# Kernel optimization log

Hardware: AMD Instinct MI355X
Metric: run time of the kernel (lower is better)

The kernel has to match this reference:

```python
import jax, jax.numpy as jnp
import numpy as np

H, HKV, D, HID, T = 16, 4, 128, 2048, 4096
THETA = 10000.0
EPS = 1e-5
NEG = -1e30


def setup_inputs() -> dict:
    key = jax.random.key(0)
    ks = jax.random.split(key, 4)
    return {
        "positions": jnp.arange(T, dtype=jnp.int32),
        "hidden_states": jax.random.normal(ks[0], (T, HID), jnp.float32),
        "w_qkv": jax.random.normal(ks[1], ((H + 2 * HKV) * D, HID), jnp.float32) * 0.02,
        "w_o": jax.random.normal(ks[2], (HID, H * D), jnp.float32) * 0.02,
        "q_norm_w": jnp.ones((H * D,), jnp.float32),
        "k_norm_w": jnp.ones((HKV * D,), jnp.float32),
    }


def _rope(pos, x):
    # x: [T, nh, D]; neox-style rotary over full head_dim
    half = D // 2
    inv_freq = 1.0 / (THETA ** (jnp.arange(0, D, 2, dtype=jnp.float32) / D))  # [D/2]
    ang = pos.astype(jnp.float32)[:, None] * inv_freq  # [T, D/2]
    cos = jnp.cos(ang)[:, None, :]
    sin = jnp.sin(ang)[:, None, :]
    x1, x2 = x[..., :half], x[..., half:]
    return jnp.concatenate([x1 * cos - x2 * sin, x2 * cos + x1 * sin], axis=-1)


def _rmsnorm(x, w):
    var = jnp.mean(x * x, axis=-1, keepdims=True)
    return x * jax.lax.rsqrt(var + EPS) * w


def reference(positions, hidden_states, w_qkv, w_o, q_norm_w, k_norm_w):
    qkv = hidden_states @ w_qkv.T  # [T, (H+2*HKV)*D]
    q, k, v = jnp.split(qkv, [H * D, H * D + HKV * D], axis=-1)
    # RoPE per head
    q = _rope(positions, q.reshape(T, H, D)).reshape(T, H * D)
    k = _rope(positions, k.reshape(T, HKV, D)).reshape(T, HKV * D)
    # QK-norm over the flattened (all-heads) q_size / kv_size, as in the module
    q = _rmsnorm(q, q_norm_w)
    k = _rmsnorm(k, k_norm_w)
    qh = q.reshape(T, H, D)
    kh = jnp.repeat(k.reshape(T, HKV, D), H // HKV, axis=1)  # GQA expand
    vh = jnp.repeat(v.reshape(T, HKV, D), H // HKV, axis=1)
    scores = jnp.einsum('qhd,khd->hqk', qh, kh) * (D ** -0.5)  # [H, T, T]
    causal = jnp.tril(jnp.ones((T, T), dtype=bool))
    scores = jnp.where(causal, scores, NEG)
    p = jax.nn.softmax(scores, axis=-1)
    attn = jnp.einsum('hqk,khd->qhd', p, vh).reshape(T, H * D)
    return attn @ w_o.T  # [T, HID]
```

## Files before the change

### kernel.cpp

```cpp
#include <hip/hip_runtime.h>
#include <hip/hip_bf16.h>

#define T_SEQ 4096
#define HID   2048
#define NH    16
#define NKV   4
#define HD    128
#define QKV_N 3072
#define QSCALE 0.12751744f
#define SMAX 24.0f

typedef unsigned short u16;
typedef __bf16 bf16x8 __attribute__((ext_vector_type(8)));
typedef float floatx4 __attribute__((ext_vector_type(4)));
typedef float floatx16 __attribute__((ext_vector_type(16)));

__device__ __forceinline__ float b2f(u16 u) {
  union { unsigned int i; float f; } x; x.i = ((unsigned int)u) << 16; return x.f;
}
__device__ __forceinline__ u16 f2b(float f) {
  union { float f; unsigned int i; } x; x.f = f;
  unsigned int i = x.i;
  unsigned int r = (i + 0x7FFFu + ((i >> 16) & 1u)) >> 16;
  return (u16)r;
}
__device__ __forceinline__ void gload_lds16(const u16* g, u16* lds) {
  __builtin_amdgcn_global_load_lds(
      (const __attribute__((address_space(1))) unsigned int*)g,
      (__attribute__((address_space(3))) unsigned int*)lds, 16, 0, 0);
}

__global__ __launch_bounds__(256) void conv_f32_bf16(const float* __restrict__ src,
                                                     u16* __restrict__ dst, int n8) {
  int i = blockIdx.x * 256 + threadIdx.x;
  if (i >= n8) return;
  const float4* s = (const float4*)(src + (size_t)i * 8);
  float4 a = s[0], b = s[1];
  union { u16 h[8]; uint4 u; } r;
  r.h[0] = f2b(a.x); r.h[1] = f2b(a.y); r.h[2] = f2b(a.z); r.h[3] = f2b(a.w);
  r.h[4] = f2b(b.x); r.h[5] = f2b(b.y); r.h[6] = f2b(b.z); r.h[7] = f2b(b.w);
  *(uint4*)(dst + (size_t)i * 8) = r.u;
}

template <int CF>
__global__ __launch_bounds__(256) void gemm_bt(const u16* __restrict__ A, int lda,
                                               const u16* __restrict__ B, int ldb,
                                               void* __restrict__ Cv, int ldc, int K) {
  __shared__ __align__(16) u16 sA[128 * 32];
  __shared__ __align__(16) u16 sB[128 * 32];
  const int tid = threadIdx.x;
  const int wave = tid >> 6, lane = tid & 63;
  const int row0 = blockIdx.y * 128, col0 = blockIdx.x * 128;
  const int wm = (wave >> 1) * 64, wn = (wave & 1) * 64;
  const int frow = lane & 15, fk = (lane >> 4) * 8;

  floatx4 acc[4][4];
#pragma unroll
  for (int i = 0; i < 4; i++)
#pragma unroll
    for (int j = 0; j < 4; j++) acc[i][j] = (floatx4){0.f, 0.f, 0.f, 0.f};

  const int c0 = wave * 2;
  const int v0 = c0 * 64 + lane;
  const int v1 = v0 + 64;
  const u16* gA0 = A + (size_t)(row0 + (v0 >> 2)) * lda + (v0 & 3) * 8;
  const u16* gA1 = A + (size_t)(row0 + (v1 >> 2)) * lda + (v1 & 3) * 8;
  const u16* gB0 = B + (size_t)(col0 + (v0 >> 2)) * ldb + (v0 & 3) * 8;
  const u16* gB1 = B + (size_t)(col0 + (v1 >> 2)) * ldb + (v1 & 3) * 8;

  for (int k0 = 0; k0 < K; k0 += 32) {
    gload_lds16(gA0 + k0, sA + c0 * 512);
    gload_lds16(gA1 + k0, sA + c0 * 512 + 512);
    gload_lds16(gB0 + k0, sB + c0 * 512);
    gload_lds16(gB1 + k0, sB + c0 * 512 + 512);
    __syncthreads();
    bf16x8 af[4], bfv[4];
#pragma unroll
    for (int i = 0; i < 4; i++) {
      af[i]  = *(const bf16x8*)(sA + (wm + i * 16 + frow) * 32 + fk);
      bfv[i] = *(const bf16x8*)(sB + (wn + i * 16 + frow) * 32 + fk);
    }
#pragma unroll
    for (int i = 0; i < 4; i++)
#pragma unroll
      for (int j = 0; j < 4; j++)
        acc[i][j] = __builtin_amdgcn_mfma_f32_16x16x32_bf16(af[i], bfv[j], acc[i][j], 0, 0, 0);
    __syncthreads();
  }
  const int crow = (lane >> 4) * 4, ccol = lane & 15;
#pragma unroll
  for (int i = 0; i < 4; i++)
#pragma unroll
    for (int j = 0; j < 4; j++)
#pragma unroll
      for (int r = 0; r < 4; r++) {
        int rr = row0 + wm + i * 16 + crow + r;
        int cc = col0 + wn + j * 16 + ccol;
        if (CF) ((float*)Cv)[(size_t)rr * ldc + cc] = acc[i][j][r];
        else    ((u16*)Cv)[(size_t)rr * ldc + cc] = f2b(acc[i][j][r]);
      }
}

__device__ __forceinline__ void fast_sincos(float ang, float* s, float* c) {
  float r = ang * 0.15915494309189535f;
  r -= floorf(r);
  *s = __builtin_amdgcn_sinf(r);
  *c = __builtin_amdgcn_cosf(r);
}

__global__ __launch_bounds__(256) void rope_norm(const int* __restrict__ pos_arr,
                                                 u16* __restrict__ qkv,
                                                 const float* __restrict__ qnw,
                                                 const float* __restrict__ knw) {
  const int t = blockIdx.x;
  const int tid = threadIdx.x;
  const int lane = tid & 63, wave = tid >> 6;
  u16* row = qkv + (size_t)t * QKV_N;
  const float pos = (float)pos_arr[t];

  float qv[8];
  float ssq = 0.f;
#pragma unroll
  for (int i = 0; i < 8; i++) {
    int e = tid * 8 + i;
    int r = e & 127, ih = e & 63;
    float invf = exp2f(-(float)ih * 0.20762050593046015f);
    float ang = pos * invf;
    float s, c;
    fast_sincos(ang, &s, &c);
    float val;
    if (r < 64) val = b2f(row[e]) * c - b2f(row[e + 64]) * s;
    else        val = b2f(row[e]) * c + b2f(row[e - 64]) * s;
    qv[i] = val;
    ssq += val * val;
  }
  float kv[2];
  float ssk = 0.f;
  const u16* krow = row + HID;
#pragma unroll
  for (int i = 0; i < 2; i++) {
    int e = tid * 2 + i;
    int r = e & 127, ih = e & 63;
    float invf = exp2f(-(float)ih * 0.20762050593046015f);
    float ang = pos * invf;
    float s, c;
    fast_sincos(ang, &s, &c);
    float val;
    if (r < 64) val = b2f(krow[e]) * c - b2f(krow[e + 64]) * s;
    else        val = b2f(krow[e]) * c + b2f(krow[e - 64]) * s;
    kv[i] = val;
    ssk += val * val;
  }
#pragma unroll
  for (int off = 1; off < 64; off <<= 1) {
    ssq += __shfl_xor(ssq, off);
    ssk += __shfl_xor(ssk, off);
  }
  __shared__ float rq[4], rk[4];
  if (lane == 0) { rq[wave] = ssq; rk[wave] = ssk; }
  __syncthreads();
  float sq = rq[0] + rq[1] + rq[2] + rq[3];
  float sk = rk[0] + rk[1] + rk[2] + rk[3];
  float qsc = rsqrtf(sq * (1.0f / 2048.0f) + 1e-5f) * QSCALE;
  float ksc = rsqrtf(sk * (1.0f / 512.0f) + 1e-5f);
#pragma unroll
  for (int i = 0; i < 8; i++) {
    int e = tid * 8 + i;
    row[e] = f2b(qv[i] * qsc * qnw[e]);
  }
#pragma unroll
  for (int i = 0; i < 2; i++) {
    int e = tid * 2 + i;
    row[HID + e] = f2b(kv[i] * ksc * knw[e]);
  }
}

__global__ __launch_bounds__(256) void transpose_v(const u16* __restrict__ qkv,
                                                   u16* __restrict__ vt) {
  __shared__ __align__(16) u16 tile[64][136];
  const int tid = threadIdx.x;
  const int h = blockIdx.y;
  const int t0 = blockIdx.x * 64;
#pragma unroll
  for (int p = 0; p < 4; p++) {
    int v = p * 256 + tid;
    int r = v >> 4, c = v & 15;
    const u16* g = qkv + (size_t)(t0 + r) * QKV_N + (HID + NKV * HD) + h * HD + c * 8;
    *(uint4*)(&tile[r][c * 8]) = *(const uint4*)g;
  }
  __syncthreads();
#pragma unroll
  for (int p = 0; p < 4; p++) {
    int v = p * 256 + tid;
    int d = v >> 3, c8 = v & 7;
    union { u16 s[8]; uint4 q; } tmp;
#pragma unroll
    for (int i = 0; i < 8; i++) tmp.s[i] = tile[c8 * 8 + i][d];
    u16* g = vt + ((size_t)h * HD + d) * T_SEQ + t0 + c8 * 8;
    *(uint4*)g = tmp.q;
  }
}

__device__ __forceinline__ void stage_kv(const u16* __restrict__ kbase,
                                         const u16* __restrict__ vbase, int kv0,
                                         u16* sk, u16* sv, int tid) {
  const int w = tid >> 6, lane = tid & 63;
#pragma unroll
  for (int i = 0; i < 4; i++) {
    int c = w * 256 + i * 64 + lane;
    int kv = c >> 4, ch = c & 15;
    const u16* g = kbase + (size_t)(kv0 + kv) * QKV_N + ((ch ^ (kv & 7)) * 8);
    gload_lds16(g, sk + (size_t)(w * 256 + i * 64) * 8);
  }
#pragma unroll
  for (int i = 0; i < 4; i++) {
    int c = w * 256 + i * 64 + lane;
    int d = c >> 3, c2 = c & 7;
    const u16* g = vbase + (size_t)d * T_SEQ + kv0 + ((c2 ^ (d & 7)) * 8);
    gload_lds16(g, sv + (size_t)(w * 256 + i * 64) * 8);
  }
}

__global__ __launch_bounds__(256, 2) void attn_kernel(u16* __restrict__ qkv,
                                                      const u16* __restrict__ vt) {
  __shared__ __align__(16) u16 sK[2][64 * 128];
  __shared__ __align__(16) u16 sV[2][128 * 64];
  __shared__ __align__(16) u16 sP[4][32 * 64];
  const int tid = threadIdx.x;
  const int wave = tid >> 6, lane = tid & 63;
  const int bid = blockIdx.x;
  int qt, h;
  if (bid < 256) { qt = bid >> 3; h = bid & 7; }
  else           { qt = 31 - ((bid & 255) >> 3); h = 8 + (bid & 7); }
  const int kvh = h >> 2;
  const int ql = lane & 31;
  const int fq2 = lane >> 5;
  const u16* kbase = qkv + HID + (size_t)kvh * HD;
  const u16* vbase = vt + (size_t)kvh * HD * T_SEQ;
  u16* sPw = sP[wave];

  const int qb = qt * 128;
  const int qw = qb + wave * 32;
  const int qmax = qw + 31;
  const int qrow = qw + ql;
  bf16x8 qf[8];
  const u16* qp = qkv + (size_t)qrow * QKV_N + h * HD + fq2 * 8;
#pragma unroll
  for (int kc = 0; kc < 8; kc++) qf[kc] = *(const bf16x8*)(qp + kc * 16);
  floatx16 O[4];
#pragma unroll
  for (int dt = 0; dt < 4; dt++)
#pragma unroll
    for (int r = 0; r < 16; r++) O[dt][r] = 0.f;
  float l_part = 0.f;

  const int nst = 2 * (qt + 1);
  stage_kv(kbase, vbase, 0, sK[0], sV[0], tid);
#pragma unroll 1
  for (int s = 0; s < nst; s++) {
    __syncthreads();
    if (s + 1 < nst)
      stage_kv(kbase, vbase, (s + 1) * 64, sK[(s + 1) & 1], sV[(s + 1) & 1], tid);
    const int kv0 = s * 64;
    if (kv0 <= qmax) {
      const u16* sk = sK[s & 1];
      const u16* sv = sV[s & 1];
      const int ntv = (kv0 + 32 <= qmax) ? 2 : 1;
#pragma unroll
      for (int nt = 0; nt < 2; nt++) {
        if (nt < ntv) {
          floatx16 S;
#pragma unroll
          for (int r = 0; r < 16; r++) S[r] = -SMAX;
#pragma unroll
          for (int kc = 0; kc < 8; kc++) {
            int ch = (kc * 2 + fq2) ^ (ql & 7);
            bf16x8 kf = *(const bf16x8*)(sk + ((nt * 32 + ql) * 16 + ch) * 8);
            S = __builtin_amdgcn_mfma_f32_32x32x16_bf16(kf, qf[kc], S, 0, 0, 0);
          }
          const bool tmask = (kv0 + nt * 32 + 31) > qw;
#pragma unroll
          for (int r = 0; r < 16; r++) {
            float v = S[r];
            if (tmask) {
              int kvg = kv0 + nt * 32 + (r & 3) + ((r >> 2) << 3) + (fq2 << 2);
              v = (kvg > qrow) ? -1e30f : v;
            }
            float p = exp2f(v);
            l_part += p;
            S[r] = p;
          }
#pragma unroll
          for (int rg = 0; rg < 4; rg++) {
            int c8 = nt * 8 + rg * 2 + fq2;
            int p8 = c8 ^ ((ql & 7) << 1);
            unsigned lo = __builtin_amdgcn_perm(__float_as_uint(S[rg * 4 + 1]),
                                                __float_as_uint(S[rg * 4 + 0]),
                                                0x07060302u);
            unsigned hi = __builtin_amdgcn_perm(__float_as_uint(S[rg * 4 + 3]),
                                                __float_as_uint(S[rg * 4 + 2]),
                                                0x07060302u);
            uint2 wv = {lo, hi};
            *(uint2*)(sPw + ql * 64 + p8 * 4) = wv;
          }
        }
      }
      asm volatile("s_waitcnt lgkmcnt(0)" ::: "memory");
      const int nc2 = min(4, ((qmax - kv0) >> 4) + 1);
#pragma unroll 1
      for (int kc2 = 0; kc2 < nc2; kc2++) {
        int c8 = (kc2 * 2 + fq2) * 2;
        int p8 = c8 ^ ((ql & 7) << 1);
        bf16x8 pf = *(const bf16x8*)(sPw + ql * 64 + p8 * 4);
#pragma unroll
        for (int dt = 0; dt < 4; dt++) {
          int ch2 = (kc2 * 2 + fq2) ^ (ql & 7);
          bf16x8 vf = *(const bf16x8*)(sv + ((dt * 32 + ql) * 8 + ch2) * 8);
          O[dt] = __builtin_amdgcn_mfma_f32_32x32x16_bf16(vf, pf, O[dt], 0, 0, 0);
        }
      }
    }
  }
  float l = l_part + __shfl_xor(l_part, 32);
  float inv = 1.0f / fmaxf(l, 1e-30f);
  u16* orow = qkv + (size_t)qrow * QKV_N + h * HD;
#pragma unroll
  for (int dt = 0; dt < 4; dt++)
#pragma unroll
    for (int rg = 0; rg < 4; rg++) {
      union { u16 hh[4]; uint2 uu; } wv;
#pragma unroll
      for (int rr = 0; rr < 4; rr++) wv.hh[rr] = f2b(O[dt][rg * 4 + rr] * inv);
      *(uint2*)(orow + dt * 32 + rg * 8 + fq2 * 4) = wv.uu;
    }
}

extern "C" void kernel_launch(void* const* d_in, const int* in_sizes, int n_in,
                              void* d_out, int out_size, void* d_ws, size_t ws_size,
                              hipStream_t stream) {
  const int* positions = (const int*)d_in[0];
  const float* hidden = (const float*)d_in[1];
  const float* w_qkv = (const float*)d_in[2];
  const float* w_o = (const float*)d_in[3];
  const float* qnw = (const float*)d_in[4];
  const float* knw = (const float*)d_in[5];
  float* out = (float*)d_out;

  u16* qkv  = (u16*)d_ws;
  u16* bufA = qkv + (size_t)T_SEQ * QKV_N;
  u16* bufB = bufA + (size_t)T_SEQ * HID;

  conv_f32_bf16<<<4096, 256, 0, stream>>>(hidden, bufA, T_SEQ * HID / 8);
  conv_f32_bf16<<<3072, 256, 0, stream>>>(w_qkv, bufB, QKV_N * HID / 8);
  gemm_bt<0><<<dim3(QKV_N / 128, T_SEQ / 128), 256, 0, stream>>>(
      bufA, HID, bufB, HID, qkv, QKV_N, HID);
  rope_norm<<<T_SEQ, 256, 0, stream>>>(positions, qkv, qnw, knw);
  conv_f32_bf16<<<2048, 256, 0, stream>>>(w_o, bufA, HID * HID / 8);
  transpose_v<<<dim3(T_SEQ / 64, NKV), 256, 0, stream>>>(qkv, bufB);
  attn_kernel<<<512, 256, 0, stream>>>(qkv, bufB);
  gemm_bt<1><<<dim3(HID / 128, T_SEQ / 128), 256, 0, stream>>>(
      qkv, QKV_N, bufA, HID, out, HID, HID);
}
```

Baseline: 434.0 us.

## Keep softmax P in registers via permlane32 swap instead of LDS round-trip

Drops the per-wave shared-memory P buffer and the store/wait/reload sequence. P is now packed to bf16 with v_cvt_pk_bf16_f32 and redistributed across lane halves with permlane32_swap, so it feeds the PV MFMA directly. The PV product is also issued per 32-key subtile, and s_setprio raises wave priority around the MFMA loops. It also swaps exp2f for the raw hardware exp2 builtin. This cuts LDS traffic and frees shared memory, at the risk of getting the register layout mapping wrong, and it loses the 16-key granularity that previously skipped fully masked PV chunks.

After: 412.2 us. 1.05x faster.

```diff
diff --git a/kernel.cpp b/kernel.cpp
--- a/kernel.cpp
+++ b/kernel.cpp
@@ -225,7 +225,6 @@
                                                       const u16* __restrict__ vt) {
   __shared__ __align__(16) u16 sK[2][64 * 128];
   __shared__ __align__(16) u16 sV[2][128 * 64];
-  __shared__ __align__(16) u16 sP[4][32 * 64];
   const int tid = threadIdx.x;
   const int wave = tid >> 6, lane = tid & 63;
   const int bid = blockIdx.x;
@@ -237,7 +236,6 @@
   const int fq2 = lane >> 5;
   const u16* kbase = qkv + HID + (size_t)kvh * HD;
   const u16* vbase = vt + (size_t)kvh * HD * T_SEQ;
-  u16* sPw = sP[wave];
 
   const int qb = qt * 128;
   const int qw = qb + wave * 32;
@@ -272,12 +270,14 @@
           floatx16 S;
 #pragma unroll
           for (int r = 0; r < 16; r++) S[r] = -SMAX;
+          __builtin_amdgcn_s_setprio(1);
 #pragma unroll
           for (int kc = 0; kc < 8; kc++) {
             int ch = (kc * 2 + fq2) ^ (ql & 7);
             bf16x8 kf = *(const bf16x8*)(sk + ((nt * 32 + ql) * 16 + ch) * 8);
             S = __builtin_amdgcn_mfma_f32_32x32x16_bf16(kf, qf[kc], S, 0, 0, 0);
           }
+          __builtin_amdgcn_s_setprio(0);
           const bool tmask = (kv0 + nt * 32 + 31) > qw;
 #pragma unroll
           for (int r = 0; r < 16; r++) {
@@ -286,37 +286,41 @@
               int kvg = kv0 + nt * 32 + (r & 3) + ((r >> 2) << 3) + (fq2 << 2);
               v = (kvg > qrow) ? -1e30f : v;
             }
-            float p = exp2f(v);
+            float p = __builtin_amdgcn_exp2f(v);
             l_part += p;
             S[r] = p;
           }
-#pragma unroll
-          for (int rg = 0; rg < 4; rg++) {
-            int c8 = nt * 8 + rg * 2 + fq2;
-            int p8 = c8 ^ ((ql & 7) << 1);
-            unsigned lo = __builtin_amdgcn_perm(__float_as_uint(S[rg * 4 + 1]),
-                                                __float_as_uint(S[rg * 4 + 0]),
-                                                0x07060302u);
-            unsigned hi = __builtin_amdgcn_perm(__float_as_uint(S[rg * 4 + 3]),
-                                                __float_as_uint(S[rg * 4 + 2]),
-                                                0x07060302u);
-            uint2 wv = {lo, hi};
-            *(uint2*)(sPw + ql * 64 + p8 * 4) = wv;
-          }
-        }
-      }
-      asm volatile("s_waitcnt lgkmcnt(0)" ::: "memory");
-      const int nc2 = min(4, ((qmax - kv0) >> 4) + 1);
-#pragma unroll 1
-      for (int kc2 = 0; kc2 < nc2; kc2++) {
-        int c8 = (kc2 * 2 + fq2) * 2;
-        int p8 = c8 ^ ((ql & 7) << 1);
-        bf16x8 pf = *(const bf16x8*)(sPw + ql * 64 + p8 * 4);
-#pragma unroll
-        for (int dt = 0; dt < 4; dt++) {
-          int ch2 = (kc2 * 2 + fq2) ^ (ql & 7);
-          bf16x8 vf = *(const bf16x8*)(sv + ((dt * 32 + ql) * 8 + ch2) * 8);
-          O[dt] = __builtin_amdgcn_mfma_f32_32x32x16_bf16(vf, pf, O[dt], 0, 0, 0);
+          unsigned cp[8];
+#pragma unroll
+          for (int i = 0; i < 8; i++) {
+            unsigned wv;
+            asm("v_cvt_pk_bf16_f32 %0, %1, %2"
+                : "=v"(wv) : "v"(S[i * 2]), "v"(S[i * 2 + 1]));
+            cp[i] = wv;
+          }
+          union { unsigned u[4]; bf16x8 v; } pf0, pf1;
+          {
+            auto r0 = __builtin_amdgcn_permlane32_swap(cp[0], cp[2], false, false);
+            pf0.u[0] = r0[0]; pf0.u[2] = r0[1];
+            auto r1 = __builtin_amdgcn_permlane32_swap(cp[1], cp[3], false, false);
+            pf0.u[1] = r1[0]; pf0.u[3] = r1[1];
+            auto r2 = __builtin_amdgcn_permlane32_swap(cp[4], cp[6], false, false);
+            pf1.u[0] = r2[0]; pf1.u[2] = r2[1];
+            auto r3 = __builtin_amdgcn_permlane32_swap(cp[5], cp[7], false, false);
+            pf1.u[1] = r3[0]; pf1.u[3] = r3[1];
+          }
+          __builtin_amdgcn_s_setprio(1);
+#pragma unroll
+          for (int c = 0; c < 2; c++) {
+            bf16x8 pf = c ? pf1.v : pf0.v;
+#pragma unroll
+            for (int dt = 0; dt < 4; dt++) {
+              int ch2 = ((nt * 2 + c) * 2 + fq2) ^ (ql & 7);
+              bf16x8 vf = *(const bf16x8*)(sv + ((dt * 32 + ql) * 8 + ch2) * 8);
+              O[dt] = __builtin_amdgcn_mfma_f32_32x32x16_bf16(vf, pf, O[dt], 0, 0, 0);
+            }
+          }
+          __builtin_amdgcn_s_setprio(0);
         }
       }
     }
```
